# Kernel tuning notes

Hardware: AMD Instinct MI355X
Metric: run time of the kernel (lower is better)

The kernel has to match this reference:

```python
import jax, jax.numpy as jnp
import numpy as np
import math

B, S, D = 2, 2048, 2048
P = 4       # num_entangled_pairs
PW = 2      # num_interference_pathways
L = 2       # num_layers
STD = 0.02
EPS = 1e-5


def _layer_norm(x, g, b):
    m = jnp.mean(x, axis=-1, keepdims=True)
    v = jnp.mean(jnp.square(x - m), axis=-1, keepdims=True)
    return (x - m) * jax.lax.rsqrt(v + EPS) * g + b


def setup_inputs() -> dict:
    key = jax.random.key(0)
    ks = jax.random.split(key, 16)
    n = lambda k, shape: jax.random.normal(k, shape, dtype=jnp.float32) * STD
    inp = {
        "x": jax.random.normal(ks[0], (B, S, D), dtype=jnp.float32),
        # superposition layer
        "amp_w": n(ks[1], (D, D)), "amp_b": jnp.zeros((D,), jnp.float32),
        "ph_w": n(ks[2], (D, D)), "ph_b": jnp.zeros((D,), jnp.float32),
        # per-layer entanglement
        "ent_w": n(ks[3], (L, D, P * D)), "ent_b": jnp.zeros((L, P * D), jnp.float32),
        "ent_pw": n(ks[4], (L, P * D, D)), "ent_pb": jnp.zeros((L, D), jnp.float32),
        # per-layer interference pathways
        "path_w": n(ks[5], (L, PW, D, D)), "path_b": jnp.zeros((L, PW, D), jnp.float32),
        "phase": jax.random.normal(ks[6], (L, PW, D), dtype=jnp.float32),
        # layer norms (norm3 / norm4 of each layer)
        "ln3_g": jnp.ones((L, D), jnp.float32), "ln3_b": jnp.zeros((L, D), jnp.float32),
        "ln4_g": jnp.ones((L, D), jnp.float32), "ln4_b": jnp.zeros((L, D), jnp.float32),
    }
    return inp


def reference(x, amp_w, amp_b, ph_w, ph_b, ent_w, ent_b, ent_pw, ent_pb,
              path_w, path_b, phase, ln3_g, ln3_b, ln4_g, ln4_b):
    # QuantumSuperpositionLayer on the input
    amp = jax.nn.sigmoid(x @ amp_w + amp_b)
    ph = jnp.tanh(x @ ph_w + ph_b) * math.pi
    h = (jnp.cos(ph) + jnp.sin(ph)) * amp                      # [B,S,D]

    for l in range(L):
        # QuantumEntanglementLayer: expand to P*D then project back
        e = h @ ent_w[l] + ent_b[l]                            # [B,S,P*D]
        ent = e @ ent_pw[l] + ent_pb[l]                        # [B,S,D]
        h = _layer_norm(h + ent, ln3_g[l], ln3_b[l])

        # QuantumInterferenceLayer: sum over pathways with phase modulation
        t = jnp.einsum('bsd,pdf->pbsf', h, path_w[l]) + path_b[l][:, None, None, :]
        mod = jnp.cos(phase[l]) + jnp.sin(phase[l])            # [PW,D]
        interf = jnp.sum(t * mod[:, None, None, :], axis=0)   # [B,S,D]
        h = _layer_norm(h + interf, ln4_g[l], ln4_b[l])
    return h
```

## Files before the change

### kernel.cpp

```cpp
#include <hip/hip_runtime.h>
#include <cstdint>
#include <cstddef>

typedef unsigned short u16;
typedef short bf16x8 __attribute__((ext_vector_type(8)));
typedef float f32x4 __attribute__((ext_vector_type(4)));

__device__ __forceinline__ float bf2f(u16 v) {
  union { unsigned int u; float f; } x; x.u = ((unsigned int)v) << 16; return x.f;
}
__device__ __forceinline__ u16 f2bf(float f) {
  union { float f; unsigned int u; } x; x.f = f;
  unsigned int r = (x.u + 0x7fffu + ((x.u >> 16) & 1u)) >> 16;
  return (u16)r;
}

__device__ __forceinline__ void async16(const u16* g, u16* lds) {
  __builtin_amdgcn_global_load_lds(
      (const __attribute__((address_space(1))) void*)g,
      (__attribute__((address_space(3))) void*)lds, 16, 0, 0);
}

#define BM 128
#define BN 128
#define BK 64

template <bool ACC>
__global__ __launch_bounds__(256) void gemm_bt(
    const u16* __restrict__ A, int lda,
    const u16* __restrict__ Bt,
    const float* __restrict__ bias,
    u16* __restrict__ C, int ldc,
    int M, int N, int K)
{
  __shared__ __align__(16) u16 As[BM * BK];
  __shared__ __align__(16) u16 Bs[BN * BK];
  const int tid = threadIdx.x;
  const int w   = tid >> 6;
  const int l   = tid & 63;
  const int bm  = blockIdx.x;
  const int bn  = blockIdx.y;
  const int wm  = w >> 1;
  const int wn  = w & 1;
  const int tRow = l & 15;
  const int quad = l >> 4;

  const u16* ag[4]; const u16* bg[4];
  u16* al[4]; u16* bl[4];
  #pragma unroll
  for (int i = 0; i < 4; ++i) {
    int s = i * 4 + w;
    int row = s * 8 + (l >> 3);
    int c   = (l & 7) ^ ((l >> 3) & 7);
    ag[i] = A  + (size_t)(bm * BM + row) * lda + c * 8;
    bg[i] = Bt + (size_t)(bn * BN + row) * K   + c * 8;
    al[i] = &As[s * 512];
    bl[i] = &Bs[s * 512];
  }

  f32x4 acc[4][4] = {};

  for (int k0 = 0; k0 < K; k0 += BK) {
    __syncthreads();
    #pragma unroll
    for (int i = 0; i < 4; ++i) {
      async16(ag[i], al[i]);
      async16(bg[i], bl[i]);
      ag[i] += BK; bg[i] += BK;
    }
    __syncthreads();
    #pragma unroll
    for (int ks = 0; ks < BK; ks += 32) {
      const int lc = (ks >> 3) + quad;
      bf16x8 af[4], bfr[4];
      #pragma unroll
      for (int mt = 0; mt < 4; ++mt) {
        int r = wm * 64 + mt * 16 + tRow;
        int p = lc ^ (tRow & 7);
        af[mt] = *(const bf16x8*)&As[r * BK + p * 8];
      }
      #pragma unroll
      for (int nt = 0; nt < 4; ++nt) {
        int r = wn * 64 + nt * 16 + tRow;
        int p = lc ^ (tRow & 7);
        bfr[nt] = *(const bf16x8*)&Bs[r * BK + p * 8];
      }
      #pragma unroll
      for (int mt = 0; mt < 4; ++mt)
        #pragma unroll
        for (int nt = 0; nt < 4; ++nt)
          acc[mt][nt] = __builtin_amdgcn_mfma_f32_16x16x32_bf16(af[mt], bfr[nt], acc[mt][nt], 0, 0, 0);
    }
  }

  const int crow0 = bm * BM + wm * 64;
  const int ccol0 = bn * BN + wn * 64;
  #pragma unroll
  for (int nt = 0; nt < 4; ++nt) {
    int col = ccol0 + nt * 16 + tRow;
    float bv = ACC ? 0.f : bias[col];
    #pragma unroll
    for (int mt = 0; mt < 4; ++mt) {
      int r0 = crow0 + mt * 16 + quad * 4;
      #pragma unroll
      for (int r = 0; r < 4; ++r) {
        size_t idx = (size_t)(r0 + r) * ldc + col;
        float v = acc[mt][nt][r] + bv;
        if (ACC) v += bf2f(C[idx]);
        C[idx] = f2bf(v);
      }
    }
  }
}

__global__ __launch_bounds__(256) void transpose_f2bf(
    const float* __restrict__ src, u16* __restrict__ dst,
    int R, int C, int srcStride, int col0)
{
  __shared__ __align__(16) u16 tile[64][72];
  const int bx = blockIdx.x;
  const int by = blockIdx.y;
  const int t = threadIdx.x;
  const int r  = t >> 4;
  const int c4 = (t & 15) * 4;
  #pragma unroll
  for (int i = 0; i < 4; ++i) {
    int row = r + i * 16;
    f32x4 v = *(const f32x4*)&src[(size_t)(by * 64 + row) * srcStride + col0 + bx * 64 + c4];
    #pragma unroll
    for (int j = 0; j < 4; ++j) tile[row][c4 + j] = f2bf(v[j]);
  }
  __syncthreads();
  const int orow0 = t >> 3;
  const int oc8   = (t & 7) * 8;
  #pragma unroll
  for (int i = 0; i < 2; ++i) {
    int orow = orow0 + i * 32;
    u16 tmp[8];
    #pragma unroll
    for (int j = 0; j < 8; ++j) tmp[j] = tile[oc8 + j][orow];
    *(uint4*)&dst[(size_t)(bx * 64 + orow) * R + by * 64 + oc8] = *(uint4*)tmp;
  }
}

__global__ void cvt_f2bf(const float* __restrict__ s, u16* __restrict__ d) {
  size_t i = ((size_t)blockIdx.x * 256 + threadIdx.x) * 8;
  f32x4 a = *(const f32x4*)&s[i];
  f32x4 b = *(const f32x4*)&s[i + 4];
  u16 o[8];
  #pragma unroll
  for (int j = 0; j < 4; ++j) { o[j] = f2bf(a[j]); o[j + 4] = f2bf(b[j]); }
  *(uint4*)&d[i] = *(uint4*)o;
}

__global__ void mod_k(const float* __restrict__ ph, float* __restrict__ m, int n) {
  int i = blockIdx.x * 256 + threadIdx.x;
  if (i < n) { float p = ph[i]; m[i] = cosf(p) + sinf(p); }
}

__global__ void concat2_k(const float* __restrict__ a, const float* __restrict__ b,
                          float* __restrict__ d, int n) {
  int i = blockIdx.x * 256 + threadIdx.x;
  if (i < n) { d[i] = a[i]; d[n + i] = b[i]; }
}

__global__ __launch_bounds__(256) void combine_path_k(
    const float* __restrict__ pw, const float* __restrict__ mod,
    u16* __restrict__ WcT, int D)
{
  __shared__ float tile[64][65];
  const int bx = blockIdx.x;
  const int by = blockIdx.y;
  const int t = threadIdx.x;
  const int r  = t >> 4;
  const int c4 = (t & 15) * 4;
  float acc[4][4];
  #pragma unroll
  for (int i = 0; i < 4; ++i)
    #pragma unroll
    for (int j = 0; j < 4; ++j) acc[i][j] = 0.f;
  for (int p = 0; p < 2; ++p) {
    float m[4];
    #pragma unroll
    for (int j = 0; j < 4; ++j) m[j] = mod[p * D + bx * 64 + c4 + j];
    #pragma unroll
    for (int i = 0; i < 4; ++i) {
      int d = by * 64 + r + i * 16;
      f32x4 v = *(const f32x4*)&pw[((size_t)p * D + d) * D + bx * 64 + c4];
      #pragma unroll
      for (int j = 0; j < 4; ++j) acc[i][j] += v[j] * m[j];
    }
  }
  #pragma unroll
  for (int i = 0; i < 4; ++i)
    #pragma unroll
    for (int j = 0; j < 4; ++j) tile[r + i * 16][c4 + j] = acc[i][j];
  __syncthreads();
  const int fo0 = t >> 3;
  const int oc8 = (t & 7) * 8;
  #pragma unroll
  for (int i = 0; i < 2; ++i) {
    int fo = fo0 + i * 32;
    u16 tmp[8];
    #pragma unroll
    for (int j = 0; j < 8; ++j) tmp[j] = f2bf(tile[oc8 + j][fo]);
    *(uint4*)&WcT[(size_t)(bx * 64 + fo) * D + by * 64 + oc8] = *(uint4*)tmp;
  }
}

__global__ void combine_bias_k(const float* __restrict__ pb, const float* __restrict__ mod,
                               float* __restrict__ bc, int D) {
  int f = blockIdx.x * 256 + threadIdx.x;
  if (f < D) bc[f] = pb[f] * mod[f] + pb[D + f] * mod[D + f];
}

__global__ __launch_bounds__(256) void superpose_k(
    const u16* __restrict__ zc, u16* __restrict__ h, int D)
{
  size_t idx = (size_t)blockIdx.x * 256 + threadIdx.x;
  int grpPerRow = D / 8;
  size_t row = idx / grpPerRow;
  int cg = (int)(idx % grpPerRow);
  size_t zbase = row * (size_t)(2 * D) + cg * 8;
  uint4 v1 = *(const uint4*)&zc[zbase];
  uint4 v2 = *(const uint4*)&zc[zbase + D];
  const u16* p1 = (const u16*)&v1;
  const u16* p2 = (const u16*)&v2;
  u16 o[8];
  #pragma unroll
  for (int j = 0; j < 8; ++j) {
    float a = bf2f(p1[j]);
    float p = bf2f(p2[j]);
    float amp = 1.f / (1.f + __expf(-a));
    float ph = 3.14159265358979323f * tanhf(p);
    float s, c;
    __sincosf(ph, &s, &c);
    o[j] = f2bf((c + s) * amp);
  }
  *(uint4*)&h[row * D + cg * 8] = *(uint4*)o;
}

template <bool F32OUT>
__global__ __launch_bounds__(256) void add_ln_k(
    const u16* __restrict__ hin, const u16* __restrict__ delta,
    const float* __restrict__ g, const float* __restrict__ b,
    void* __restrict__ outp, int D)
{
  const int row = blockIdx.x;
  const int t = threadIdx.x;
  const size_t base = (size_t)row * D;
  uint4 hv = *(const uint4*)&hin[base + t * 8];
  uint4 dv = *(const uint4*)&delta[base + t * 8];
  const u16* hp = (const u16*)&hv;
  const u16* dp = (const u16*)&dv;
  float x[8];
  float s = 0.f, s2 = 0.f;
  #pragma unroll
  for (int j = 0; j < 8; ++j) {
    x[j] = bf2f(hp[j]) + bf2f(dp[j]);
    s += x[j]; s2 += x[j] * x[j];
  }
  #pragma unroll
  for (int o = 32; o > 0; o >>= 1) {
    s  += __shfl_down(s, o, 64);
    s2 += __shfl_down(s2, o, 64);
  }
  __shared__ float ss[4], ss2[4];
  if ((t & 63) == 0) { ss[t >> 6] = s; ss2[t >> 6] = s2; }
  __syncthreads();
  float S  = ss[0] + ss[1] + ss[2] + ss[3];
  float S2 = ss2[0] + ss2[1] + ss2[2] + ss2[3];
  float mean = S / D;
  float var = S2 / D - mean * mean;
  float rstd = rsqrtf(var + 1e-5f);
  float y[8];
  #pragma unroll
  for (int j = 0; j < 8; ++j)
    y[j] = (x[j] - mean) * rstd * g[t * 8 + j] + b[t * 8 + j];
  if constexpr (F32OUT) {
    float* out = (float*)outp;
    f32x4 lo = {y[0], y[1], y[2], y[3]};
    f32x4 hi = {y[4], y[5], y[6], y[7]};
    *(f32x4*)&out[base + t * 8]     = lo;
    *(f32x4*)&out[base + t * 8 + 4] = hi;
  } else {
    u16* out = (u16*)outp;
    u16 o8[8];
    #pragma unroll
    for (int j = 0; j < 8; ++j) o8[j] = f2bf(y[j]);
    *(uint4*)&out[base + t * 8] = *(uint4*)o8;
  }
}

extern "C" void kernel_launch(void* const* d_in, const int* in_sizes, int n_in,
                              void* d_out, int out_size, void* d_ws, size_t ws_size,
                              hipStream_t stream) {
  const float* x      = (const float*)d_in[0];
  const float* amp_w  = (const float*)d_in[1];
  const float* amp_b  = (const float*)d_in[2];
  const float* ph_w   = (const float*)d_in[3];
  const float* ph_b   = (const float*)d_in[4];
  const float* ent_w  = (const float*)d_in[5];
  const float* ent_b  = (const float*)d_in[6];
  const float* ent_pw = (const float*)d_in[7];
  const float* ent_pb = (const float*)d_in[8];
  const float* path_w = (const float*)d_in[9];
  const float* path_b = (const float*)d_in[10];
  const float* phase  = (const float*)d_in[11];
  const float* ln3_g  = (const float*)d_in[12];
  const float* ln3_b  = (const float*)d_in[13];
  const float* ln4_g  = (const float*)d_in[14];
  const float* ln4_b  = (const float*)d_in[15];

  constexpr int D = 2048, PD = 8192, M = 4096, L = 2, PW = 2;
  constexpr int HPD = PD / 2;

  char* p = (char*)d_ws;
  float* modf = (float*)p; p += (size_t)L * PW * D * sizeof(float);
  float* bcf  = (float*)p; p += (size_t)2 * D * sizeof(float);
  p = (char*)d_ws + 65536;
  u16* h  = (u16*)p; p += (size_t)M * D * sizeof(u16);
  u16* t1 = (u16*)p; p += (size_t)M * D * sizeof(u16);
  u16* wT = (u16*)p; p += (size_t)HPD * D * sizeof(u16);
  u16* e  = (u16*)p; p += (size_t)M * PD * sizeof(u16);

  u16* xb = e;
  u16* zc = e + (size_t)M * D;

  dim3 b256(256);

  mod_k<<<(L * PW * D) / 256, b256, 0, stream>>>(phase, modf, L * PW * D);
  cvt_f2bf<<<(M * D) / (256 * 8), b256, 0, stream>>>(x, xb);

  transpose_f2bf<<<dim3(D / 64, D / 64), b256, 0, stream>>>(amp_w, wT, D, D, D, 0);
  transpose_f2bf<<<dim3(D / 64, D / 64), b256, 0, stream>>>(ph_w, wT + (size_t)D * D, D, D, D, 0);
  concat2_k<<<D / 256, b256, 0, stream>>>(amp_b, ph_b, bcf, D);
  gemm_bt<false><<<dim3(M / BM, (2 * D) / BN), b256, 0, stream>>>(
      xb, D, wT, bcf, zc, 2 * D, M, 2 * D, D);
  superpose_k<<<(M * D) / (256 * 8), b256, 0, stream>>>(zc, h, D);

  for (int l = 0; l < L; ++l) {
    for (int s = 0; s < 2; ++s) {
      transpose_f2bf<<<dim3(HPD / 64, D / 64), b256, 0, stream>>>(
          ent_w + (size_t)l * D * PD, wT, D, HPD, PD, s * HPD);
      gemm_bt<false><<<dim3(M / BM, HPD / BN), b256, 0, stream>>>(
          h, D, wT, ent_b + (size_t)l * PD + s * HPD, e + s * HPD, PD, M, HPD, D);
    }
    for (int s = 0; s < 2; ++s) {
      transpose_f2bf<<<dim3(D / 64, HPD / 64), b256, 0, stream>>>(
          ent_pw + (size_t)l * PD * D + (size_t)s * HPD * D, wT, HPD, D, D, 0);
      if (s == 0)
        gemm_bt<false><<<dim3(M / BM, D / BN), b256, 0, stream>>>(
            e, PD, wT, ent_pb + (size_t)l * D, t1, D, M, D, HPD);
      else
        gemm_bt<true><<<dim3(M / BM, D / BN), b256, 0, stream>>>(
            e + HPD, PD, wT, bcf , t1, D, M, D, HPD);
    }
    add_ln_k<false><<<M, b256, 0, stream>>>(h, t1, ln3_g + (size_t)l * D, ln3_b + (size_t)l * D, h, D);
    combine_path_k<<<dim3(D / 64, D / 64), b256, 0, stream>>>(
        path_w + (size_t)l * PW * D * D, modf + (size_t)l * PW * D, wT, D);
    combine_bias_k<<<D / 256, b256, 0, stream>>>(path_b + (size_t)l * PW * D, modf + (size_t)l * PW * D, bcf, D);
    gemm_bt<false><<<dim3(M / BM, D / BN), b256, 0, stream>>>(
        h, D, wT, bcf, t1, D, M, D, D);
    if (l == L - 1)
      add_ln_k<true><<<M, b256, 0, stream>>>(h, t1, ln4_g + (size_t)l * D, ln4_b + (size_t)l * D, d_out, D);
    else
      add_ln_k<false><<<M, b256, 0, stream>>>(h, t1, ln4_g + (size_t)l * D, ln4_b + (size_t)l * D, h, D);
  }
}
```

Before: 1.296 ms.

## Rewrite GEMM as 256x256 double-buffered 8-wave pipelined kernel

The bf16 GEMM moves from 128x128 tiles with 4 waves and a single LDS buffer to 256x256 tiles with 8 waves and double-buffered LDS. Global-to-LDS async loads for the next K-slice are split into quarters and interleaved with MFMA blocks, using explicit vmcnt waits, barriers and s_setprio around the MFMA groups. The goal is to hide memory latency and raise data reuse per tile. In exchange the kernel uses 128 KB of LDS and more registers, and the larger tiles leave fewer blocks per launch, which risks poorer occupancy and load balance.

```diff
diff --git a/kernel.cpp b/kernel.cpp
--- a/kernel.cpp
+++ b/kernel.cpp
@@ -21,91 +21,153 @@
       (__attribute__((address_space(3))) void*)lds, 16, 0, 0);
 }
 
-#define BM 128
-#define BN 128
+#define BM 256
+#define BN 256
 #define BK 64
 
+#define VMW(n) asm volatile("s_waitcnt vmcnt(" #n ")" ::: "memory")
+#define BAR() do { asm volatile("" ::: "memory"); \
+                   __builtin_amdgcn_s_barrier(); \
+                   asm volatile("" ::: "memory"); } while (0)
+
 template <bool ACC>
-__global__ __launch_bounds__(256) void gemm_bt(
+__global__ __launch_bounds__(512, 2) void gemm_bt(
     const u16* __restrict__ A, int lda,
     const u16* __restrict__ Bt,
     const float* __restrict__ bias,
     u16* __restrict__ C, int ldc,
     int M, int N, int K)
 {
-  __shared__ __align__(16) u16 As[BM * BK];
-  __shared__ __align__(16) u16 Bs[BN * BK];
+  __shared__ __align__(16) u16 As[2][BM * BK];
+  __shared__ __align__(16) u16 Bs[2][BN * BK];
   const int tid = threadIdx.x;
   const int w   = tid >> 6;
   const int l   = tid & 63;
-  const int bm  = blockIdx.x;
-  const int bn  = blockIdx.y;
-  const int wm  = w >> 1;
-  const int wn  = w & 1;
+  const int wm  = w >> 2;
+  const int wn  = w & 3;
   const int tRow = l & 15;
   const int quad = l >> 4;
-
-  const u16* ag[4]; const u16* bg[4];
-  u16* al[4]; u16* bl[4];
-  #pragma unroll
-  for (int i = 0; i < 4; ++i) {
-    int s = i * 4 + w;
-    int row = s * 8 + (l >> 3);
-    int c   = (l & 7) ^ ((l >> 3) & 7);
-    ag[i] = A  + (size_t)(bm * BM + row) * lda + c * 8;
-    bg[i] = Bt + (size_t)(bn * BN + row) * K   + c * 8;
-    al[i] = &As[s * 512];
-    bl[i] = &Bs[s * 512];
-  }
-
-  f32x4 acc[4][4] = {};
-
-  for (int k0 = 0; k0 < K; k0 += BK) {
-    __syncthreads();
-    #pragma unroll
-    for (int i = 0; i < 4; ++i) {
-      async16(ag[i], al[i]);
-      async16(bg[i], bl[i]);
-      ag[i] += BK; bg[i] += BK;
+  const int s7 = tRow & 7;
+  const int bm = blockIdx.x, bn = blockIdx.y;
+
+  const int rsub = tid >> 3;
+  const int cLog = (tid & 7) ^ (rsub & 7);
+  const u16* ag[2][2]; const u16* bg[2][2];
+  #pragma unroll
+  for (int H = 0; H < 2; ++H) {
+    #pragma unroll
+    for (int j = 0; j < 2; ++j) {
+      const int ra = H * 64 + j * 128 + rsub;
+      ag[H][j] = A + (size_t)(bm * BM + ra) * lda + cLog * 8;
+      const int p  = j * 64 + rsub;
+      const int rb = (p & 31) + H * 32 + (p >> 5) * 64;
+      bg[H][j] = Bt + (size_t)(bn * BN + rb) * K + cLog * 8;
     }
-    __syncthreads();
-    #pragma unroll
-    for (int ks = 0; ks < BK; ks += 32) {
-      const int lc = (ks >> 3) + quad;
-      bf16x8 af[4], bfr[4];
-      #pragma unroll
-      for (int mt = 0; mt < 4; ++mt) {
-        int r = wm * 64 + mt * 16 + tRow;
-        int p = lc ^ (tRow & 7);
-        af[mt] = *(const bf16x8*)&As[r * BK + p * 8];
-      }
-      #pragma unroll
-      for (int nt = 0; nt < 4; ++nt) {
-        int r = wn * 64 + nt * 16 + tRow;
-        int p = lc ^ (tRow & 7);
-        bfr[nt] = *(const bf16x8*)&Bs[r * BK + p * 8];
-      }
-      #pragma unroll
-      for (int mt = 0; mt < 4; ++mt)
-        #pragma unroll
-        for (int nt = 0; nt < 4; ++nt)
-          acc[mt][nt] = __builtin_amdgcn_mfma_f32_16x16x32_bf16(af[mt], bfr[nt], acc[mt][nt], 0, 0, 0);
-    }
-  }
-
-  const int crow0 = bm * BM + wm * 64;
+  }
+  const int ldsW = w * 512;
+
+  f32x4 acc[8][4] = {};
+  bf16x8 af[4][2], bf0[2][2], bf1[2][2];
+
+#define STAGE_A(H, NB) do { \
+    async16(ag[H][0], &As[NB][(H) * 8192 + ldsW]); \
+    async16(ag[H][1], &As[NB][(H) * 8192 + 4096 + ldsW]); \
+    ag[H][0] += BK; ag[H][1] += BK; } while (0)
+#define STAGE_B(H, NB) do { \
+    async16(bg[H][0], &Bs[NB][(H) * 8192 + ldsW]); \
+    async16(bg[H][1], &Bs[NB][(H) * 8192 + 4096 + ldsW]); \
+    bg[H][0] += BK; bg[H][1] += BK; } while (0)
+#define READ_A(CB, H) do { \
+    _Pragma("unroll") \
+    for (int mt = 0; mt < 4; ++mt) { \
+      _Pragma("unroll") \
+      for (int kk = 0; kk < 2; ++kk) \
+        af[mt][kk] = *(const bf16x8*)&As[CB][(H) * 8192 + \
+            (wm * 64 + mt * 16 + tRow) * 64 + (((kk * 4 + quad) ^ s7)) * 8]; \
+    } } while (0)
+#define READ_B(CB, H, BF) do { \
+    _Pragma("unroll") \
+    for (int nt = 0; nt < 2; ++nt) { \
+      _Pragma("unroll") \
+      for (int kk = 0; kk < 2; ++kk) \
+        BF[nt][kk] = *(const bf16x8*)&Bs[CB][(H) * 8192 + \
+            (wn * 32 + nt * 16 + tRow) * 64 + (((kk * 4 + quad) ^ s7)) * 8]; \
+    } } while (0)
+#define MFMA_BLK(BF, MI0, NI0) do { \
+    __builtin_amdgcn_s_setprio(1); \
+    _Pragma("unroll") \
+    for (int mt = 0; mt < 4; ++mt) { \
+      _Pragma("unroll") \
+      for (int nt = 0; nt < 2; ++nt) { \
+        _Pragma("unroll") \
+        for (int kk = 0; kk < 2; ++kk) \
+          acc[(MI0) + mt][(NI0) + nt] = __builtin_amdgcn_mfma_f32_16x16x32_bf16( \
+              af[mt][kk], BF[nt][kk], acc[(MI0) + mt][(NI0) + nt], 0, 0, 0); \
+      } } \
+    __builtin_amdgcn_s_setprio(0); } while (0)
+
+  STAGE_A(0, 0); STAGE_B(0, 0); STAGE_B(1, 0); STAGE_A(1, 0);
+  VMW(4);
+  BAR();
+
+  const int NT = K / BK;
+  for (int u = 0; u < NT - 1; ++u) {
+    const int cb = u & 1, nb = cb ^ 1;
+    READ_A(cb, 0); READ_B(cb, 0, bf0);
+    STAGE_A(0, nb);
+    VMW(4); BAR();
+    MFMA_BLK(bf0, 0, 0);
+    BAR();
+    READ_B(cb, 1, bf1);
+    STAGE_B(0, nb);
+    VMW(4); BAR();
+    MFMA_BLK(bf1, 0, 2);
+    BAR();
+    READ_A(cb, 1);
+    STAGE_B(1, nb);
+    VMW(4); BAR();
+    MFMA_BLK(bf1, 4, 2);
+    BAR();
+    STAGE_A(1, nb);
+    VMW(4); BAR();
+    MFMA_BLK(bf0, 4, 0);
+    BAR();
+  }
+  {
+    const int cb = (NT - 1) & 1;
+    READ_A(cb, 0); READ_B(cb, 0, bf0);
+    VMW(2); BAR();
+    MFMA_BLK(bf0, 0, 0);
+    BAR();
+    READ_B(cb, 1, bf1);
+    VMW(0); BAR();
+    MFMA_BLK(bf1, 0, 2);
+    BAR();
+    READ_A(cb, 1);
+    BAR();
+    MFMA_BLK(bf1, 4, 2);
+    BAR();
+    MFMA_BLK(bf0, 4, 0);
+  }
+#undef STAGE_A
+#undef STAGE_B
+#undef READ_A
+#undef READ_B
+#undef MFMA_BLK
+
+  const int crow0 = bm * BM + wm * 128;
   const int ccol0 = bn * BN + wn * 64;
   #pragma unroll
-  for (int nt = 0; nt < 4; ++nt) {
-    int col = ccol0 + nt * 16 + tRow;
+  for (int ni = 0; ni < 4; ++ni) {
+    int col = ccol0 + ni * 16 + tRow;
     float bv = ACC ? 0.f : bias[col];
     #pragma unroll
-    for (int mt = 0; mt < 4; ++mt) {
-      int r0 = crow0 + mt * 16 + quad * 4;
+    for (int mi = 0; mi < 8; ++mi) {
+      int r0 = crow0 + mi * 16 + quad * 4;
       #pragma unroll
       for (int r = 0; r < 4; ++r) {
         size_t idx = (size_t)(r0 + r) * ldc + col;
-        float v = acc[mt][nt][r] + bv;
+        float v = acc[mi][ni][r] + bv;
         if (ACC) v += bf2f(C[idx]);
         C[idx] = f2bf(v);
       }
@@ -328,6 +390,7 @@
   u16* zc = e + (size_t)M * D;
 
   dim3 b256(256);
+  dim3 b512(512);
 
   mod_k<<<(L * PW * D) / 256, b256, 0, stream>>>(phase, modf, L * PW * D);
   cvt_f2bf<<<(M * D) / (256 * 8), b256, 0, stream>>>(x, xb);
@@ -335,7 +398,7 @@
   transpose_f2bf<<<dim3(D / 64, D / 64), b256, 0, stream>>>(amp_w, wT, D, D, D, 0);
   transpose_f2bf<<<dim3(D / 64, D / 64), b256, 0, stream>>>(ph_w, wT + (size_t)D * D, D, D, D, 0);
   concat2_k<<<D / 256, b256, 0, stream>>>(amp_b, ph_b, bcf, D);
-  gemm_bt<false><<<dim3(M / BM, (2 * D) / BN), b256, 0, stream>>>(
+  gemm_bt<false><<<dim3(M / BM, (2 * D) / BN), b512, 0, stream>>>(
       xb, D, wT, bcf, zc, 2 * D, M, 2 * D, D);
   superpose_k<<<(M * D) / (256 * 8), b256, 0, stream>>>(zc, h, D);
 
@@ -343,24 +406,24 @@
     for (int s = 0; s < 2; ++s) {
       transpose_f2bf<<<dim3(HPD / 64, D / 64), b256, 0, stream>>>(
           ent_w + (size_t)l * D * PD, wT, D, HPD, PD, s * HPD);
-      gemm_bt<false><<<dim3(M / BM, HPD / BN), b256, 0, stream>>>(
+      gemm_bt<false><<<dim3(M / BM, HPD / BN), b512, 0, stream>>>(
           h, D, wT, ent_b + (size_t)l * PD + s * HPD, e + s * HPD, PD, M, HPD, D);
     }
     for (int s = 0; s < 2; ++s) {
       transpose_f2bf<<<dim3(D / 64, HPD / 64), b256, 0, stream>>>(
           ent_pw + (size_t)l * PD * D + (size_t)s * HPD * D, wT, HPD, D, D, 0);
       if (s == 0)
-        gemm_bt<false><<<dim3(M / BM, D / BN), b256, 0, stream>>>(
+        gemm_bt<false><<<dim3(M / BM, D / BN), b512, 0, stream>>>(
             e, PD, wT, ent_pb + (size_t)l * D, t1, D, M, D, HPD);
       else
-        gemm_bt<true><<<dim3(M / BM, D / BN), b256, 0, stream>>>(
+        gemm_bt<true><<<dim3(M / BM, D / BN), b512, 0, stream>>>(
             e + HPD, PD, wT, bcf , t1, D, M, D, HPD);
     }
     add_ln_k<false><<<M, b256, 0, stream>>>(h, t1, ln3_g + (size_t)l * D, ln3_b + (size_t)l * D, h, D);
     combine_path_k<<<dim3(D / 64, D / 64), b256, 0, stream>>>(
         path_w + (size_t)l * PW * D * D, modf + (size_t)l * PW * D, wT, D);
     combine_bias_k<<<D / 256, b256, 0, stream>>>(path_b + (size_t)l * PW * D, modf + (size_t)l * PW * D, bcf, D);
-    gemm_bt<false><<<dim3(M / BM, D / BN), b256, 0, stream>>>(
+    gemm_bt<false><<<dim3(M / BM, D / BN), b512, 0, stream>>>(
         h, D, wT, bcf, t1, D, M, D, D);
     if (l == L - 1)
       add_ln_k<true><<<M, b256, 0, stream>>>(h, t1, ln4_g + (size_t)l * D, ln4_b + (size_t)l * D, d_out, D);
```

Result: slower. 1.511 ms (+16.6%).
